# Performance work log

Measured on AMD Instinct MI355X. Metric: run time of the kernel, lower is better.

The kernel has to match this reference:

```python
import jax, jax.numpy as jnp
import numpy as np

D, L, H = 10000, 512, 1024
B = 8

def setup_inputs() -> dict:
    key = jax.random.key(0)
    k1, k2, k3 = jax.random.split(key, 3)
    vocab = jax.random.normal(k1, (D, H), dtype=jnp.float32)
    description = jax.random.normal(k2, (B, L, H), dtype=jnp.float32)
    default_embedding = jax.random.uniform(k3, (H,), dtype=jnp.float32)
    return {"vocab": vocab, "description": description, "default_embedding": default_embedding}

def reference(vocab, description, default_embedding):
    # full_vocab: (D+1, H) -- concept vocab plus learned default embedding
    full_vocab = jnp.concatenate([vocab, default_embedding[None, :]], axis=0)
    # logits: (B, L, D+1) = tokens @ full_vocab.T (broadcast over batch, no repeat needed)
    logits = jnp.einsum('blh,dh->bld', description, full_vocab)
    similarity = jax.nn.softmax(logits, axis=2)
    # blend: default-slot weight times raw tokens + concept-weighted vocab mix
    concept_based = similarity[:, :, -1:] * description + jnp.einsum('bld,dh->blh', similarity[:, :, :-1], vocab)
    return (concept_based, similarity)
```

## Files before the change

### kernel.cpp

```cpp
#include <hip/hip_runtime.h>
#include <stdint.h>

#define D_    10000
#define DP1   10001
#define NPAD2 10240
#define H_    1024
#define BL    4096
#define NPB   160
#define CANDS 1024
#define GC    512

typedef float  f32x4  __attribute__((ext_vector_type(4)));
typedef __bf16 bf16x8 __attribute__((ext_vector_type(8)));
typedef unsigned short u16;
typedef u16    u16x8  __attribute__((ext_vector_type(8)));

__device__ __forceinline__ u16 f2bf(float x) {
    union { float f; unsigned u; } v; v.f = x;
    unsigned r = v.u + 0x7FFFu + ((v.u >> 16) & 1u);
    return (u16)(r >> 16);
}

#define GLOAD_LDS16(gsrc, ldst)                                             \
    __builtin_amdgcn_global_load_lds(                                       \
        (__attribute__((address_space(1))) void*)(void*)(gsrc),             \
        (__attribute__((address_space(3))) void*)(void*)(ldst), 16, 0, 0)


__global__ __launch_bounds__(256)
void split_desc_k(const float* __restrict__ desc, u16* __restrict__ hi) {
    size_t i = ((size_t)blockIdx.x * 256 + threadIdx.x) * 8;
    f32x4 x0 = *(const f32x4*)(desc + i);
    f32x4 x1 = *(const f32x4*)(desc + i + 4);
    u16x8 h;
#pragma unroll
    for (int e = 0; e < 4; e++) { h[e] = f2bf(x0[e]); h[4 + e] = f2bf(x1[e]); }
    *(u16x8*)(hi + i) = h;
}

__global__ __launch_bounds__(256)
void split_fv_k(const float* __restrict__ vocab, const float* __restrict__ defe,
                u16* __restrict__ hi) {
    size_t i = ((size_t)blockIdx.x * 256 + threadIdx.x) * 8;
    int d = (int)(i >> 10);
    f32x4 x0 = {0.f, 0.f, 0.f, 0.f}, x1 = {0.f, 0.f, 0.f, 0.f};
    if (d < D_) {
        x0 = *(const f32x4*)(vocab + i);
        x1 = *(const f32x4*)(vocab + i + 4);
    } else if (d == D_) {
        int h = (int)(i & 1023);
        x0 = *(const f32x4*)(defe + h);
        x1 = *(const f32x4*)(defe + h + 4);
    }
    u16x8 h8;
#pragma unroll
    for (int e = 0; e < 4; e++) { h8[e] = f2bf(x0[e]); h8[4 + e] = f2bf(x1[e]); }
    *(u16x8*)(hi + i) = h8;
}


#define G1_MFMA(a, b, c) __builtin_amdgcn_mfma_f32_16x16x32_bf16((a), (b), (c), 0, 0, 0)

#define G1_STAGE(AhB, BhB, kk) do {                                         \
    GLOAD_LDS16(a_h  + (kk), (char*)(AhB) + tid16);                         \
    GLOAD_LDS16(b_h0 + (kk), (char*)(BhB) + tid16);                         \
    GLOAD_LDS16(b_h1 + (kk), (char*)(BhB) + tid16 + 8192);                  \
} while (0)

#define G1_ITER(AhB, BhB, t) do {                                           \
    bf16x8 afh[4], bfh[4];                                                  \
    _Pragma("unroll")                                                       \
    for (int i = 0; i < 4; i++) {                                           \
        afh[i] = *(const bf16x8*)&AhB[aoff[i]];                             \
        bfh[i] = *(const bf16x8*)&BhB[boff[i]];                             \
    }                                                                       \
    __builtin_amdgcn_s_setprio(1);                                          \
    _Pragma("unroll")                                                       \
    for (int i = 0; i < 2; i++)                                             \
        _Pragma("unroll")                                                   \
        for (int j = 0; j < 4; j++)                                         \
            acc[i][j] = G1_MFMA(afh[i], bfh[j], acc[i][j]);                 \
    __builtin_amdgcn_s_setprio(0);                                          \
    asm volatile("s_waitcnt lgkmcnt(0)" ::: "memory");                      \
    __builtin_amdgcn_s_barrier();                                           \
    if ((t) + 2 < 32) G1_STAGE(AhB, BhB, ((t) + 2) * 32);                   \
    __builtin_amdgcn_s_setprio(1);                                          \
    _Pragma("unroll")                                                       \
    for (int i = 2; i < 4; i++)                                             \
        _Pragma("unroll")                                                   \
        for (int j = 0; j < 4; j++)                                         \
            acc[i][j] = G1_MFMA(afh[i], bfh[j], acc[i][j]);                 \
    __builtin_amdgcn_s_setprio(0);                                          \
    if ((t) + 2 < 32)      asm volatile("s_waitcnt vmcnt(3)" ::: "memory"); \
    else if ((t) + 1 < 32) asm volatile("s_waitcnt vmcnt(0)" ::: "memory"); \
    __builtin_amdgcn_s_barrier();                                           \
} while (0)

__global__ __launch_bounds__(512, 2)
void gemm1_k(const u16* __restrict__ Ahg, const u16* __restrict__ Bhg,
             float* __restrict__ C, float* __restrict__ Pt) {
    __shared__ u16 Ah0[128 * 32], Bh0[256 * 32];
    __shared__ u16 Ah1[128 * 32], Bh1[256 * 32];

    const int tid  = threadIdx.x;
    const int wave = tid >> 6, lane = tid & 63;
    const int wr = wave >> 2, wc = wave & 3;
    const int quad = lane >> 4, r16 = lane & 15;
    const int m0 = blockIdx.y * 128, n0 = blockIdx.x * 256;

    f32x4 zero = {0.f, 0.f, 0.f, 0.f};
    f32x4 acc[4][4];
#pragma unroll
    for (int i = 0; i < 4; i++)
#pragma unroll
        for (int j = 0; j < 4; j++) acc[i][j] = zero;

    const int arow = tid >> 2, achk = tid & 3;
    const int ascol = (achk ^ ((arow >> 1) & 3)) * 8;
    const u16* a_h = Ahg + (size_t)(m0 + arow) * H_ + ascol;
    const int brow0 = arow,        bscol0 = (achk ^ ((brow0 >> 1) & 3)) * 8;
    const int brow1 = 128 + arow,  bscol1 = (achk ^ ((brow1 >> 1) & 3)) * 8;
    const u16* b_h0 = Bhg + (size_t)(n0 + brow0) * H_ + bscol0;
    const u16* b_h1 = Bhg + (size_t)(n0 + brow1) * H_ + bscol1;
    const int tid16 = tid * 16;
    const int aswz = (r16 >> 1) & 3;

    int aoff[4], boff[4];
#pragma unroll
    for (int i = 0; i < 4; i++) {
        aoff[i] = (wr * 64 + i * 16 + r16) * 32 + ((quad ^ aswz) * 8);
        boff[i] = (wc * 64 + i * 16 + r16) * 32 + ((quad ^ aswz) * 8);
    }

    G1_STAGE(Ah0, Bh0, 0);
    G1_STAGE(Ah1, Bh1, 32);
    asm volatile("s_waitcnt vmcnt(3)" ::: "memory");
    __builtin_amdgcn_s_barrier();

    for (int t = 0; t < 32; t += 2) {
        G1_ITER(Ah0, Bh0, t);
        G1_ITER(Ah1, Bh1, t + 1);
    }

#pragma unroll
    for (int i = 0; i < 4; i++) {
        int gm = m0 + wr * 64 + i * 16 + quad * 4;
#pragma unroll
        for (int j = 0; j < 4; j++) {
            int gn = n0 + wc * 64 + j * 16 + r16;
            if (gn < DP1) {
#pragma unroll
                for (int reg = 0; reg < 4; reg++)
                    C[(size_t)(gm + reg) * DP1 + gn] = acc[i][j][reg];
            }
        }
    }
    const int pcol = blockIdx.x * 4 + wc;
#pragma unroll
    for (int i = 0; i < 4; i++) {
#pragma unroll
        for (int reg = 0; reg < 4; reg++) {
            float m = -3.4e38f;
#pragma unroll
            for (int j = 0; j < 4; j++) {
                int gn = n0 + wc * 64 + j * 16 + r16;
                if (gn < DP1) m = fmaxf(m, acc[i][j][reg]);
            }
#pragma unroll
            for (int off = 1; off < 16; off <<= 1)
                m = fmaxf(m, __shfl_xor(m, off, 64));
            float s = 0.f;
#pragma unroll
            for (int j = 0; j < 4; j++) {
                int gn = n0 + wc * 64 + j * 16 + r16;
                if (gn < DP1) s += __expf(acc[i][j][reg] - m);
            }
#pragma unroll
            for (int off = 1; off < 16; off <<= 1)
                s += __shfl_xor(s, off, 64);
            if (r16 == 0) {
                int grow = m0 + wr * 64 + i * 16 + quad * 4 + reg;
                float2 v; v.x = m; v.y = s;
                *(float2*)(Pt + ((size_t)grow * NPB + pcol) * 2) = v;
            }
        }
    }
}

__global__ __launch_bounds__(256)
void softmax_finish_k(float* __restrict__ sim, const float* __restrict__ Pt,
                      const float* __restrict__ vocab, const float* __restrict__ defe,
                      const float* __restrict__ desc, float* __restrict__ out) {
    __shared__ float red[8];
    __shared__ int   cnt;
    __shared__ int   cidx[GC];
    __shared__ float lex[GC + 1];
    __shared__ float psh[GC + 1];
    const int tid = threadIdx.x;
    const int row = blockIdx.x;
    float* rowp = sim + (size_t)row * DP1;
    const float* drow = desc + (size_t)row * H_;
    const int lane = tid & 63, wv = tid >> 6;
    if (tid == 0) cnt = 0;

    float pm = -3.4e38f, ps = 0.f;
    if (tid < NPB) {
        float2 v = *(const float2*)(Pt + ((size_t)row * NPB + tid) * 2);
        pm = v.x; ps = v.y;
    }
    float mt = pm;
#pragma unroll
    for (int off = 32; off; off >>= 1) mt = fmaxf(mt, __shfl_down(mt, off, 64));
    if (lane == 0) red[wv] = mt;
    __syncthreads();
    const float M = fmaxf(fmaxf(red[0], red[1]), fmaxf(red[2], red[3]));
    float zt = (tid < NPB) ? __expf(pm - M) * ps : 0.f;
#pragma unroll
    for (int off = 32; off; off >>= 1) zt += __shfl_down(zt, off, 64);
    if (lane == 0) red[4 + wv] = zt;
    __syncthreads();
    const float Z = red[4] + red[5] + red[6] + red[7];
    const float invZ = 1.f / Z;

#pragma unroll
    for (int s = 0; s < 9; s++) {
        f32x4 l = *(const f32x4*)(rowp + s * 1024 + tid * 4);
        f32x4 p;
#pragma unroll
        for (int e = 0; e < 4; e++) p[e] = __expf(l[e] - M) * invZ;
        *(f32x4*)(rowp + s * 1024 + tid * 4) = p;
#pragma unroll
        for (int e = 0; e < 4; e++)
            if (p[e] > 1e-8f) {
                int k = atomicAdd(&cnt, 1);
                if (k < GC) cidx[k] = s * 1024 + tid * 4 + e;
            }
    }
    {
        const int base = 9216 + tid * 4;
#pragma unroll
        for (int e = 0; e < 4; e++) {
            int idx = base + e;
            if (idx <= D_) {
                float p = __expf(rowp[idx] - M) * invZ;
                rowp[idx] = p;
                if (idx < D_ && p > 1e-8f) {
                    int k = atomicAdd(&cnt, 1);
                    if (k < GC) cidx[k] = idx;
                }
            }
        }
    }
    __syncthreads();

    const int cnt0 = cnt;
    const bool ovf = cnt0 > GC;
    const int cc = ovf ? GC : cnt0;
    if (!ovf) {
        for (int c = wv; c <= cc; c += 4) {
            const float* vrow = (c == cc) ? defe : (vocab + (size_t)cidx[c] * H_);
            float s = 0.f;
#pragma unroll
            for (int q = 0; q < 4; q++) {
                f32x4 dv = *(const f32x4*)(drow + (q * 64 + lane) * 4);
                f32x4 vv = *(const f32x4*)(vrow + (q * 64 + lane) * 4);
                s += dv[0] * vv[0] + dv[1] * vv[1] + dv[2] * vv[2] + dv[3] * vv[3];
            }
#pragma unroll
            for (int off = 32; off; off >>= 1) s += __shfl_down(s, off, 64);
            if (lane == 0) lex[c] = s;
        }
        __syncthreads();
        float m2 = -3.4e38f;
        for (int c = 0; c <= cc; c++) m2 = fmaxf(m2, lex[c]);
        float Z2 = 0.f;
        for (int c = 0; c <= cc; c++) Z2 += __expf(lex[c] - m2);
        const float iZ2 = 1.f / Z2;
        for (int i = tid; i <= cc; i += 256) psh[i] = __expf(lex[i] - m2) * iZ2;
        __syncthreads();
        for (int c = tid; c < cc; c += 256) rowp[cidx[c]] = psh[c];
        if (tid == 0) rowp[D_] = psh[cc];

        f32x4 a = psh[cc] * ((const f32x4*)drow)[tid];
        for (int c = 0; c < cc; c++)
            a += psh[c] * ((const f32x4*)(vocab + (size_t)cidx[c] * H_))[tid];
        ((f32x4*)(out + (size_t)row * H_))[tid] = a;
    } else {
        f32x4 a = rowp[D_] * ((const f32x4*)drow)[tid];
        for (int d = 0; d < D_; d++) {
            float p = rowp[d];
            if (p > 1e-8f) a += p * ((const f32x4*)(vocab + (size_t)d * H_))[tid];
        }
        ((f32x4*)(out + (size_t)row * H_))[tid] = a;
    }
}

__global__ __launch_bounds__(256)
void naive_logits_k(const float* __restrict__ vocab, const float* __restrict__ desc,
                    const float* __restrict__ defe, float* __restrict__ sim) {
    int d = blockIdx.x * 256 + threadIdx.x;
    if (d >= DP1) return;
    const float* vr = (d < D_) ? (vocab + (size_t)d * H_) : defe;
    const float* dr = desc + (size_t)blockIdx.y * H_;
    float s = 0.f;
    for (int h = 0; h < H_; h++) s = fmaf(dr[h], vr[h], s);
    sim[(size_t)blockIdx.y * DP1 + d] = s;
}

__global__ __launch_bounds__(1024)
void softmax_gather_k(float* __restrict__ sim, const float* __restrict__ vocab,
                      const float* __restrict__ desc, float* __restrict__ out) {
    __shared__ float red[16];
    __shared__ float wslot;
    __shared__ int   cnt;
    __shared__ int   cidx[CANDS];
    __shared__ float cp[CANDS];
    const int tid = threadIdx.x;
    const int row = blockIdx.x;
    float* rowp = sim + (size_t)row * DP1;
    if (tid == 0) cnt = 0;

    const int a0 = (4 - (row & 3)) & 3;
    const int b0 = a0 + tid * 4;
    const int b1 = a0 + 4096 + tid * 4;
    const int b2 = a0 + 8192 + tid * 4;

    float vh = (tid < a0) ? rowp[tid] : -3.4e38f;
    f32x4 v0 = *(const f32x4*)(rowp + b0);
    f32x4 v1 = *(const f32x4*)(rowp + b1);
    f32x4 v2;
    if (b2 + 3 <= D_) {
        v2 = *(const f32x4*)(rowp + b2);
    } else {
#pragma unroll
        for (int e = 0; e < 4; e++)
            v2[e] = (b2 + e <= D_) ? rowp[b2 + e] : -3.4e38f;
    }

    float mx = vh;
#pragma unroll
    for (int e = 0; e < 4; e++) mx = fmaxf(mx, fmaxf(v0[e], fmaxf(v1[e], v2[e])));
#pragma unroll
    for (int off = 32; off; off >>= 1) mx = fmaxf(mx, __shfl_down(mx, off, 64));
    if ((tid & 63) == 0) red[tid >> 6] = mx;
    __syncthreads();
#pragma unroll
    for (int w = 0; w < 16; w++) mx = fmaxf(mx, red[w]);

    float s0 = 0.f;
    vh = __expf(vh - mx); s0 += vh;
#pragma unroll
    for (int e = 0; e < 4; e++) {
        v0[e] = __expf(v0[e] - mx); s0 += v0[e];
        v1[e] = __expf(v1[e] - mx); s0 += v1[e];
        v2[e] = __expf(v2[e] - mx); s0 += v2[e];
    }
#pragma unroll
    for (int off = 32; off; off >>= 1) s0 += __shfl_down(s0, off, 64);
    __syncthreads();
    if ((tid & 63) == 0) red[tid >> 6] = s0;
    __syncthreads();
    float sum = 0.f;
#pragma unroll
    for (int w = 0; w < 16; w++) sum += red[w];
    const float inv = 1.f / sum;
    const float thr = sum * 1e-7f;

    if (tid < a0) {
        float p = vh * inv;
        rowp[tid] = p;
        if (vh > thr) {
            int k = atomicAdd(&cnt, 1);
            if (k < CANDS) { cidx[k] = tid; cp[k] = p; }
        }
    }
    {
        f32x4 p0 = v0 * inv;
        *(f32x4*)(rowp + b0) = p0;
#pragma unroll
        for (int e = 0; e < 4; e++)
            if (v0[e] > thr) {
                int k = atomicAdd(&cnt, 1);
                if (k < CANDS) { cidx[k] = b0 + e; cp[k] = p0[e]; }
            }
        f32x4 p1 = v1 * inv;
        *(f32x4*)(rowp + b1) = p1;
#pragma unroll
        for (int e = 0; e < 4; e++)
            if (v1[e] > thr) {
                int k = atomicAdd(&cnt, 1);
                if (k < CANDS) { cidx[k] = b1 + e; cp[k] = p1[e]; }
            }
#pragma unroll
        for (int e = 0; e < 4; e++) {
            int idx = b2 + e;
            if (idx <= D_) {
                float p = v2[e] * inv;
                rowp[idx] = p;
                if (idx == D_) wslot = p;
                else if (v2[e] > thr) {
                    int k = atomicAdd(&cnt, 1);
                    if (k < CANDS) { cidx[k] = idx; cp[k] = p; }
                }
            }
        }
    }
    __syncthreads();

    const float w = wslot;
    float a = w * desc[(size_t)row * H_ + tid];
    if (cnt <= CANDS) {
        const int k = cnt;
        for (int c = 0; c < k; c++)
            a += cp[c] * vocab[(size_t)cidx[c] * H_ + tid];
    } else {
        const float pthr = thr * inv;
        for (int d = 0; d < D_; d++) {
            float p = rowp[d];
            if (p > pthr) a += p * vocab[(size_t)d * H_ + tid];
        }
    }
    out[(size_t)row * H_ + tid] = a;
}

extern "C" void kernel_launch(void* const* d_in, const int* in_sizes, int n_in,
                              void* d_out, int out_size, void* d_ws, size_t ws_size,
                              hipStream_t stream) {
    (void)in_sizes; (void)n_in; (void)out_size;
    const float* vocab = (const float*)d_in[0];
    const float* desc  = (const float*)d_in[1];
    const float* defe  = (const float*)d_in[2];
    float* out = (float*)d_out;
    float* sim = out + (size_t)BL * H_;

    const size_t REQ = 34603008ull;
    char* ws = (char*)d_ws;

    if (ws_size >= REQ) {
        u16*   dhi = (u16*)(ws + 0);
        u16*   fhi = (u16*)(ws + 8388608);
        float* Pt  = (float*)(ws + 29360128);

        split_desc_k<<<2048, 256, 0, stream>>>(desc, dhi);
        split_fv_k<<<5120, 256, 0, stream>>>(vocab, defe, fhi);
        gemm1_k<<<dim3(40, 32), 512, 0, stream>>>(dhi, fhi, sim, Pt);
        softmax_finish_k<<<4096, 256, 0, stream>>>(sim, Pt, vocab, defe, desc, out);
    } else {
        naive_logits_k<<<dim3(40, BL), 256, 0, stream>>>(vocab, desc, defe, sim);
        softmax_gather_k<<<4096, 1024, 0, stream>>>(sim, vocab, desc, out);
    }
}
```

Before: 410.6 us.

## Split softmax finish into row-stat, parallel prob-stream and gather kernels

The fused per-row softmax/gather kernel is broken into three kernels. A small row-statistics kernel computes the max and 1/Z. A 2D-grid streaming kernel turns logits into probabilities and collects candidate indices through per-row global atomics. A gather kernel then does the sparse vocab blend. The two bf16 conversion kernels are also merged into a single launch. The aim is more parallelism for the memory-bound probability rewrite and fewer launches before the GEMM, at the cost of extra launches, global atomics and a workspace round-trip for the candidate lists.

```diff
diff --git a/kernel.cpp b/kernel.cpp
--- a/kernel.cpp
+++ b/kernel.cpp
@@ -28,34 +28,35 @@
 
 
 __global__ __launch_bounds__(256)
-void split_desc_k(const float* __restrict__ desc, u16* __restrict__ hi) {
-    size_t i = ((size_t)blockIdx.x * 256 + threadIdx.x) * 8;
-    f32x4 x0 = *(const f32x4*)(desc + i);
-    f32x4 x1 = *(const f32x4*)(desc + i + 4);
-    u16x8 h;
-#pragma unroll
-    for (int e = 0; e < 4; e++) { h[e] = f2bf(x0[e]); h[4 + e] = f2bf(x1[e]); }
-    *(u16x8*)(hi + i) = h;
-}
-
-__global__ __launch_bounds__(256)
-void split_fv_k(const float* __restrict__ vocab, const float* __restrict__ defe,
-                u16* __restrict__ hi) {
-    size_t i = ((size_t)blockIdx.x * 256 + threadIdx.x) * 8;
-    int d = (int)(i >> 10);
-    f32x4 x0 = {0.f, 0.f, 0.f, 0.f}, x1 = {0.f, 0.f, 0.f, 0.f};
-    if (d < D_) {
-        x0 = *(const f32x4*)(vocab + i);
-        x1 = *(const f32x4*)(vocab + i + 4);
-    } else if (d == D_) {
-        int h = (int)(i & 1023);
-        x0 = *(const f32x4*)(defe + h);
-        x1 = *(const f32x4*)(defe + h + 4);
-    }
-    u16x8 h8;
-#pragma unroll
-    for (int e = 0; e < 4; e++) { h8[e] = f2bf(x0[e]); h8[4 + e] = f2bf(x1[e]); }
-    *(u16x8*)(hi + i) = h8;
+void split_all_k(const float* __restrict__ desc, const float* __restrict__ vocab,
+                 const float* __restrict__ defe,
+                 u16* __restrict__ dhi, u16* __restrict__ fhi) {
+    const int b = blockIdx.x;
+    if (b < 2048) {
+        size_t i = ((size_t)b * 256 + threadIdx.x) * 8;
+        f32x4 x0 = *(const f32x4*)(desc + i);
+        f32x4 x1 = *(const f32x4*)(desc + i + 4);
+        u16x8 h;
+#pragma unroll
+        for (int e = 0; e < 4; e++) { h[e] = f2bf(x0[e]); h[4 + e] = f2bf(x1[e]); }
+        *(u16x8*)(dhi + i) = h;
+    } else {
+        size_t i = ((size_t)(b - 2048) * 256 + threadIdx.x) * 8;
+        int d = (int)(i >> 10);
+        f32x4 x0 = {0.f, 0.f, 0.f, 0.f}, x1 = {0.f, 0.f, 0.f, 0.f};
+        if (d < D_) {
+            x0 = *(const f32x4*)(vocab + i);
+            x1 = *(const f32x4*)(vocab + i + 4);
+        } else if (d == D_) {
+            int h = (int)(i & 1023);
+            x0 = *(const f32x4*)(defe + h);
+            x1 = *(const f32x4*)(defe + h + 4);
+        }
+        u16x8 h8;
+#pragma unroll
+        for (int e = 0; e < 4; e++) { h8[e] = f2bf(x0[e]); h8[4 + e] = f2bf(x1[e]); }
+        *(u16x8*)(fhi + i) = h8;
+    }
 }
 
 
@@ -188,56 +189,49 @@
 }
 
 __global__ __launch_bounds__(256)
-void softmax_finish_k(float* __restrict__ sim, const float* __restrict__ Pt,
-                      const float* __restrict__ vocab, const float* __restrict__ defe,
-                      const float* __restrict__ desc, float* __restrict__ out) {
-    __shared__ float red[8];
-    __shared__ int   cnt;
-    __shared__ int   cidx[GC];
-    __shared__ float lex[GC + 1];
-    __shared__ float psh[GC + 1];
-    const int tid = threadIdx.x;
-    const int row = blockIdx.x;
+void rowstat_k(const float* __restrict__ Pt, float2* __restrict__ stats,
+               int* __restrict__ gcnt) {
+    const int tid = threadIdx.x, lane = tid & 63, wv = tid >> 6;
+    const int row = blockIdx.x * 4 + wv;
+    const float2* pp = (const float2*)Pt + (size_t)row * NPB;
+    float2 p0 = pp[lane];
+    float2 p1 = pp[lane + 64];
+    float2 p2 = (lane < 32) ? pp[lane + 128] : p0;
+    float m = fmaxf(fmaxf(p0.x, p1.x), p2.x);
+#pragma unroll
+    for (int off = 32; off; off >>= 1) m = fmaxf(m, __shfl_xor(m, off, 64));
+    float z = __expf(p0.x - m) * p0.y + __expf(p1.x - m) * p1.y;
+    if (lane < 32) z += __expf(p2.x - m) * p2.y;
+#pragma unroll
+    for (int off = 32; off; off >>= 1) z += __shfl_xor(z, off, 64);
+    if (lane == 0) {
+        float2 st; st.x = m; st.y = 1.f / z;
+        stats[row] = st;
+        gcnt[row] = 0;
+    }
+}
+
+__global__ __launch_bounds__(256)
+void prob_stream_k(float* __restrict__ sim, const float2* __restrict__ stats,
+                   int* __restrict__ gcnt, int* __restrict__ gcidx) {
+    const int row = blockIdx.y;
+    const float2 st = stats[row];
+    const float M = st.x, invZ = st.y;
     float* rowp = sim + (size_t)row * DP1;
-    const float* drow = desc + (size_t)row * H_;
-    const int lane = tid & 63, wv = tid >> 6;
-    if (tid == 0) cnt = 0;
-
-    float pm = -3.4e38f, ps = 0.f;
-    if (tid < NPB) {
-        float2 v = *(const float2*)(Pt + ((size_t)row * NPB + tid) * 2);
-        pm = v.x; ps = v.y;
-    }
-    float mt = pm;
-#pragma unroll
-    for (int off = 32; off; off >>= 1) mt = fmaxf(mt, __shfl_down(mt, off, 64));
-    if (lane == 0) red[wv] = mt;
-    __syncthreads();
-    const float M = fmaxf(fmaxf(red[0], red[1]), fmaxf(red[2], red[3]));
-    float zt = (tid < NPB) ? __expf(pm - M) * ps : 0.f;
-#pragma unroll
-    for (int off = 32; off; off >>= 1) zt += __shfl_down(zt, off, 64);
-    if (lane == 0) red[4 + wv] = zt;
-    __syncthreads();
-    const float Z = red[4] + red[5] + red[6] + red[7];
-    const float invZ = 1.f / Z;
-
-#pragma unroll
-    for (int s = 0; s < 9; s++) {
-        f32x4 l = *(const f32x4*)(rowp + s * 1024 + tid * 4);
+    const int base = blockIdx.x * 1024 + threadIdx.x * 4;
+    if (base + 3 <= D_) {
+        f32x4 l = *(const f32x4*)(rowp + base);
         f32x4 p;
 #pragma unroll
         for (int e = 0; e < 4; e++) p[e] = __expf(l[e] - M) * invZ;
-        *(f32x4*)(rowp + s * 1024 + tid * 4) = p;
+        *(f32x4*)(rowp + base) = p;
 #pragma unroll
         for (int e = 0; e < 4; e++)
-            if (p[e] > 1e-8f) {
-                int k = atomicAdd(&cnt, 1);
-                if (k < GC) cidx[k] = s * 1024 + tid * 4 + e;
-            }
-    }
-    {
-        const int base = 9216 + tid * 4;
+            if (p[e] > 1e-8f && base + e < D_) {
+                int k = atomicAdd(&gcnt[row], 1);
+                if (k < GC) gcidx[(size_t)row * GC + k] = base + e;
+            }
+    } else if (base <= D_) {
 #pragma unroll
         for (int e = 0; e < 4; e++) {
             int idx = base + e;
@@ -245,17 +239,34 @@
                 float p = __expf(rowp[idx] - M) * invZ;
                 rowp[idx] = p;
                 if (idx < D_ && p > 1e-8f) {
-                    int k = atomicAdd(&cnt, 1);
-                    if (k < GC) cidx[k] = idx;
+                    int k = atomicAdd(&gcnt[row], 1);
+                    if (k < GC) gcidx[(size_t)row * GC + k] = idx;
                 }
             }
         }
     }
-    __syncthreads();
-
-    const int cnt0 = cnt;
+}
+
+__global__ __launch_bounds__(256)
+void gather_k(float* __restrict__ sim, const int* __restrict__ gcnt,
+              const int* __restrict__ gcidx,
+              const float* __restrict__ vocab, const float* __restrict__ defe,
+              const float* __restrict__ desc, float* __restrict__ out) {
+    __shared__ int   cidx[GC];
+    __shared__ float lex[GC + 1];
+    __shared__ float psh[GC + 1];
+    const int tid = threadIdx.x;
+    const int row = blockIdx.x;
+    const int cnt0 = gcnt[row];
     const bool ovf = cnt0 > GC;
     const int cc = ovf ? GC : cnt0;
+    float* rowp = sim + (size_t)row * DP1;
+    const float* drow = desc + (size_t)row * H_;
+    const int lane = tid & 63, wv = tid >> 6;
+
+    for (int c = tid; c < cc; c += 256) cidx[c] = gcidx[(size_t)row * GC + c];
+    __syncthreads();
+
     if (!ovf) {
         for (int c = wv; c <= cc; c += 4) {
             const float* vrow = (c == cc) ? defe : (vocab + (size_t)cidx[c] * H_);
@@ -433,18 +444,22 @@
     float* out = (float*)d_out;
     float* sim = out + (size_t)BL * H_;
 
-    const size_t REQ = 34603008ull;
+    const size_t REQ = 43040768ull;
     char* ws = (char*)d_ws;
 
     if (ws_size >= REQ) {
-        u16*   dhi = (u16*)(ws + 0);
-        u16*   fhi = (u16*)(ws + 8388608);
-        float* Pt  = (float*)(ws + 29360128);
-
-        split_desc_k<<<2048, 256, 0, stream>>>(desc, dhi);
-        split_fv_k<<<5120, 256, 0, stream>>>(vocab, defe, fhi);
+        u16*    dhi   = (u16*)(ws + 0);
+        u16*    fhi   = (u16*)(ws + 8388608);
+        float*  Pt    = (float*)(ws + 29360128);
+        int*    gcnt  = (int*)(ws + 34603008);
+        int*    gcidx = (int*)(ws + 34619392);
+        float2* stats = (float2*)(ws + 43008000);
+
+        split_all_k<<<7168, 256, 0, stream>>>(desc, vocab, defe, dhi, fhi);
         gemm1_k<<<dim3(40, 32), 512, 0, stream>>>(dhi, fhi, sim, Pt);
-        softmax_finish_k<<<4096, 256, 0, stream>>>(sim, Pt, vocab, defe, desc, out);
+        rowstat_k<<<1024, 256, 0, stream>>>(Pt, stats, gcnt);
+        prob_stream_k<<<dim3(10, 4096), 256, 0, stream>>>(sim, stats, gcnt, gcidx);
+        gather_k<<<4096, 256, 0, stream>>>(sim, gcnt, gcidx, vocab, defe, desc, out);
     } else {
         naive_logits_k<<<dim3(40, BL), 256, 0, stream>>>(vocab, desc, defe, sim);
         softmax_gather_k<<<4096, 1024, 0, stream>>>(sim, vocab, desc, out);
```

New measurement: 409.5 us. About the same (-0.3%).
